# Optimization experiments

Measured on AMD Instinct MI355X. Metric: run time of the kernel, lower is better.

## Reference

```python
import jax, jax.numpy as jnp
import numpy as np

HEAD_DIM = 64


def rotate_half(x):
    x1, x2 = jnp.split(x, 2, axis=-1)
    return jnp.concatenate((-x2, x1), axis=-1)


def setup_inputs() -> dict:
    key = jax.random.key(0)
    ks = jax.random.split(key, 12)
    B, S, H, Hkv, D, hid = 1, 1536, 64, 8, HEAD_DIM, 2880
    std = 0.02
    x = jax.random.normal(ks[0], (B, S, hid), jnp.float32)
    # real RoPE cache, layout [cos | sin] of shape (S, 2*D)
    inv = 1.0 / (10000.0 ** (np.arange(0, D, 2, dtype=np.float32) / D))
    freqs = np.outer(np.arange(S, dtype=np.float32), inv)          # (S, D/2)
    emb = np.concatenate([freqs, freqs], axis=-1)                  # (S, D)
    rope_cache = jnp.asarray(
        np.concatenate([np.cos(emb), np.sin(emb)], axis=-1), jnp.float32
    )
    return {
        "x": x,
        "rope_cache": rope_cache,
        "wq_w": jax.random.normal(ks[1], (H * D, hid), jnp.float32) * std,
        "wq_b": jax.random.normal(ks[2], (H * D,), jnp.float32) * std,
        "wk_w": jax.random.normal(ks[3], (Hkv * D, hid), jnp.float32) * std,
        "wk_b": jax.random.normal(ks[4], (Hkv * D,), jnp.float32) * std,
        "wv_w": jax.random.normal(ks[5], (Hkv * D, hid), jnp.float32) * std,
        "wv_b": jax.random.normal(ks[6], (Hkv * D,), jnp.float32) * std,
        "wo_w": jax.random.normal(ks[7], (hid, H * D), jnp.float32) * std,
        "wo_b": jax.random.normal(ks[8], (hid,), jnp.float32) * std,
        "sinks": jax.random.normal(ks[9], (H,), jnp.float32) * std,
    }


def reference(x, rope_cache, wq_w, wq_b, wk_w, wk_b, wv_w, wv_b, wo_w, wo_b, sinks):
    B, S, hid = x.shape
    D = HEAD_DIM
    H = wq_w.shape[0] // D
    Hkv = wk_w.shape[0] // D
    n_rep = H // Hkv

    q = (x @ wq_w.T + wq_b).reshape(B, S, H, D)
    k = (x @ wk_w.T + wk_b).reshape(B, S, Hkv, D)
    v = (x @ wv_w.T + wv_b).reshape(B, S, Hkv, D)

    # RoPE (rotate-half form); rope_cache[:, :D]=cos, [:, D:]=sin
    cos = rope_cache[:S, :D][None, :, None, :]
    sin = rope_cache[:S, D:][None, :, None, :]
    q = q * cos + rotate_half(q) * sin
    k = k * cos + rotate_half(k) * sin

    # GQA repeat_kv: interleaved repeat along head dim
    k = jnp.repeat(k, n_rep, axis=2)  # (B, S, H, D)
    v = jnp.repeat(v, n_rep, axis=2)

    scale = 1.0 / jnp.sqrt(jnp.asarray(D, x.dtype))
    scores = jnp.einsum("bqhd,bkhd->bhqk", q, k) * scale  # (B, H, S, S)
    i = jnp.arange(S)
    causal = i[:, None] >= i[None, :]
    neg = jnp.asarray(jnp.finfo(scores.dtype).min, scores.dtype)
    scores = jnp.where(causal[None, None], scores, neg)

    lse = jax.nn.logsumexp(scores, axis=-1)               # (B, H, S)
    attn = jax.nn.softmax(scores, axis=-1)
    out = jnp.einsum("bhqk,bkhd->bqhd", attn, v)          # (B, S, H, D)

    # attention-sink rescale: sigmoid(lse - sink_logit)
    sink_scale = jax.nn.sigmoid(lse - sinks[None, :, None])  # (B, H, S)
    out = out * jnp.transpose(sink_scale, (0, 2, 1))[..., None]

    out = out.reshape(B, S, H * D)
    return out @ wo_w.T + wo_b
```

## Files before the change

kernel.cpp:

```cpp
#include <hip/hip_runtime.h>

typedef unsigned short u16;
typedef unsigned int u32;
typedef __attribute__((ext_vector_type(8))) __bf16 bf16x8;
typedef __attribute__((ext_vector_type(8))) u16 u16x8;
typedef __attribute__((ext_vector_type(4))) u16 u16x4;
typedef __attribute__((ext_vector_type(4))) float f32x4;
typedef __attribute__((ext_vector_type(2))) u32 u32x2;

#define DEV static __device__ __forceinline__

DEV u16 f2bf(float f) {
  unsigned u = __builtin_bit_cast(unsigned, f);
  u += 0x7FFFu + ((u >> 16) & 1u);
  return (u16)(u >> 16);
}

DEV float ex2(float x) { return __builtin_amdgcn_exp2f(x); }

DEV u32 cvt_pk_bf16(float lo, float hi) {
  u32 r;
  asm("v_cvt_pk_bf16_f32 %0, %1, %2" : "=v"(r) : "v"(lo), "v"(hi));
  return r;
}

DEV f32x4 mfma16(bf16x8 a, bf16x8 b, f32x4 c) {
  return __builtin_amdgcn_mfma_f32_16x16x32_bf16(a, b, c, 0, 0, 0);
}

DEV f32x4 fmax4(f32x4 a, f32x4 b) {
  f32x4 r;
  r[0] = fmaxf(a[0], b[0]); r[1] = fmaxf(a[1], b[1]);
  r[2] = fmaxf(a[2], b[2]); r[3] = fmaxf(a[3], b[3]);
  return r;
}

DEV void gload_lds16(const u16* g, u16* lds) {
  __builtin_amdgcn_global_load_lds(
      (const __attribute__((address_space(1))) void*)g,
      (__attribute__((address_space(3))) void*)lds, 16, 0, 0);
}

DEV void vm_wait4() { asm volatile("s_waitcnt vmcnt(4)" ::: "memory"); }
DEV void vm_wait2() { asm volatile("s_waitcnt vmcnt(2)" ::: "memory"); }
DEV void vm_wait0() { asm volatile("s_waitcnt vmcnt(0)" ::: "memory"); }

__global__ __launch_bounds__(256) void cvt_all(
    const float* __restrict__ x, const float* __restrict__ wq,
    const float* __restrict__ wk, const float* __restrict__ wv,
    const float* __restrict__ wo, const float* __restrict__ qb,
    const float* __restrict__ kb, const float* __restrict__ vb,
    u16* __restrict__ x_bf, u16* __restrict__ wqkv_bf,
    u16* __restrict__ wo_bf, float* __restrict__ bias_p) {
  const int NX = 1536 * 2880 / 8;
  const int NWQ = 4096 * 2880 / 8;
  const int NWKV = 512 * 2880 / 8;
  const int NWO = 3072 * 4096 / 8;
  const int C0 = NX, C1 = C0 + NWQ, C2 = C1 + NWKV, C3 = C2 + NWKV;
  const int C4 = C3 + NWO, C5 = C4 + 5120 / 8;
  int i = blockIdx.x * 256 + threadIdx.x;
  if (i >= C5) return;
  if (i < C4) {
    const float* s;
    u16* d;
    bool pad = false;
    if (i < C0) { s = x + (size_t)i * 8; d = x_bf + (size_t)i * 8; }
    else if (i < C1) { size_t q = i - C0; s = wq + q * 8; d = wqkv_bf + q * 8; }
    else if (i < C2) { size_t q = i - C1; s = wk + q * 8; d = wqkv_bf + (size_t)NWQ * 8 + q * 8; }
    else if (i < C3) { size_t q = i - C2; s = wv + q * 8; d = wqkv_bf + (size_t)(NWQ + NWKV) * 8 + q * 8; }
    else {
      size_t q = i - C3;
      int row = (int)(q >> 9);
      pad = (row >= 2880);
      s = wo + q * 8; d = wo_bf + q * 8;
    }
    u16x8 o;
    if (!pad) {
      float4 v0 = *(const float4*)s;
      float4 v1 = *(const float4*)(s + 4);
      o = (u16x8){f2bf(v0.x), f2bf(v0.y), f2bf(v0.z), f2bf(v0.w),
                  f2bf(v1.x), f2bf(v1.y), f2bf(v1.z), f2bf(v1.w)};
    } else {
      o = (u16x8){0, 0, 0, 0, 0, 0, 0, 0};
    }
    *(u16x8*)d = o;
  } else {
    int e = (i - C4) * 8;
#pragma unroll
    for (int j = 0; j < 8; j++) {
      int idx = e + j;
      bias_p[idx] = (idx < 4096) ? qb[idx] : (idx < 4608 ? kb[idx - 4096] : vb[idx - 4608]);
    }
  }
}

template <int MODE>
__global__ __launch_bounds__(512) void gemm128(const u16* __restrict__ A,
                                               const u16* __restrict__ B,
                                               const float* __restrict__ bias,
                                               float* __restrict__ C,
                                               u16* __restrict__ Obf,
                                               const float* __restrict__ rope,
                                               int M, int K, int Nreal, int ldc) {
  __shared__ u16 smA[2][128 * 64];
  __shared__ u16 smB[2][128 * 64];
  int nbm = M >> 7;
  int chunk = gridDim.x >> 3;
  int wg = (blockIdx.x & 7) * chunk + (blockIdx.x >> 3);
  int bm = wg % nbm, bn = wg / nbm;
  int t = threadIdx.x, lane = t & 63, wv = t >> 6;
  int wr = wv >> 1, wc = wv & 1;
  int l15 = lane & 15, hi = lane >> 4;
  f32x4 acc[2][4] = {};
  int tr = t >> 3;
  int scol = ((t & 7) ^ (tr & 7)) * 8;
  const u16* Ab = A + (size_t)(bm * 128 + tr) * K + scol;
  const u16* Bb = B + (size_t)(bn * 128 + tr) * K + scol;

  auto stage = [&](int b, int ks) {
    int k0 = ks * 64;
    gload_lds16(Ab + k0, &smA[b][t * 8]);
    gload_lds16(Ab + k0 + (size_t)64 * K, &smA[b][4096 + t * 8]);
    gload_lds16(Bb + k0, &smB[b][t * 8]);
    gload_lds16(Bb + k0 + (size_t)64 * K, &smB[b][4096 + t * 8]);
  };

  int NK = K >> 6;
  stage(0, 0);
  stage(1, 1);
  for (int ks = 0; ks < NK; ks++) {
    int cur = ks & 1;
    if (ks + 1 < NK) vm_wait4(); else vm_wait0();
    __builtin_amdgcn_s_barrier();
    __builtin_amdgcn_sched_barrier(0);
#pragma unroll
    for (int kk = 0; kk < 2; kk++) {
      int sc = ((kk * 4 + hi) ^ (l15 & 7)) * 8;
      bf16x8 af[2], bfr[4];
#pragma unroll
      for (int m = 0; m < 2; m++)
        af[m] = *(const bf16x8*)(&smA[cur][(wr * 32 + m * 16 + l15) * 64 + sc]);
#pragma unroll
      for (int n = 0; n < 4; n++)
        bfr[n] = *(const bf16x8*)(&smB[cur][(wc * 64 + n * 16 + l15) * 64 + sc]);
      __builtin_amdgcn_s_setprio(1);
#pragma unroll
      for (int m = 0; m < 2; m++)
#pragma unroll
        for (int n = 0; n < 4; n++)
          acc[m][n] = mfma16(af[m], bfr[n], acc[m][n]);
      __builtin_amdgcn_s_setprio(0);
    }
    __builtin_amdgcn_s_barrier();
    if (ks + 2 < NK) stage(cur, ks + 2);
  }

  int r0 = bm * 128 + wr * 32 + hi * 4;
  int c0 = bn * 128 + wc * 64 + l15;
  if (MODE == 0) {
#pragma unroll
    for (int n = 0; n < 4; n++) {
      int col = c0 + n * 16;
      if (col >= Nreal) continue;
      float bv = bias[col];
#pragma unroll
      for (int m = 0; m < 2; m++)
#pragma unroll
        for (int r = 0; r < 4; r++)
          C[(size_t)(r0 + m * 16 + r) * ldc + col] = acc[m][n][r] + bv;
    }
  } else {
    float bv[4];
#pragma unroll
    for (int n = 0; n < 4; n++) bv[n] = bias[c0 + n * 16];
    if (bn < 36) {
      float scale = (bn < 32) ? 0.180336880f : 1.0f;
#pragma unroll
      for (int m = 0; m < 2; m++) {
#pragma unroll
        for (int r = 0; r < 4; r++) {
          int s = r0 + m * 16 + r;
          const float* rp = rope + (size_t)s * 128;
          float cv0 = rp[l15], cv1 = rp[l15 + 16];
          float sv0 = rp[64 + l15], sv1 = rp[64 + l15 + 16];
          float v0 = acc[0][0][r], v1 = acc[0][1][r];
          float v2 = acc[0][2][r], v3 = acc[0][3][r];
          if (m) { v0 = acc[1][0][r]; v1 = acc[1][1][r]; v2 = acc[1][2][r]; v3 = acc[1][3][r]; }
          v0 += bv[0]; v1 += bv[1]; v2 += bv[2]; v3 += bv[3];
          u16* po = Obf + (size_t)s * 5120 + c0;
          po[0]  = f2bf((v0 * cv0 - v2 * sv0) * scale);
          po[16] = f2bf((v1 * cv1 - v3 * sv1) * scale);
          po[32] = f2bf((v2 * cv0 + v0 * sv0) * scale);
          po[48] = f2bf((v3 * cv1 + v1 * sv1) * scale);
        }
      }
    } else {
#pragma unroll
      for (int m = 0; m < 2; m++)
#pragma unroll
        for (int r = 0; r < 4; r++) {
          int s = r0 + m * 16 + r;
          u16* po = Obf + (size_t)s * 5120 + c0;
#pragma unroll
          for (int n = 0; n < 4; n++) po[n * 16] = f2bf(acc[m][n][r] + bv[n]);
        }
    }
  }
}

__global__ __launch_bounds__(256) void cast_trT(const u16* __restrict__ src,
                                                u16* __restrict__ dst, int S, int Hkv,
                                                int ld, int col0) {
  __shared__ u16 tile[64][65];
  int s0 = blockIdx.x * 64;
  int hkv = blockIdx.y;
  int t = threadIdx.x;
  int dl = (t & 15) * 4;
  int sl = t >> 4;
#pragma unroll
  for (int j = 0; j < 4; j++) {
    int s = sl + j * 16;
    u16x4 v = *(const u16x4*)(src + (size_t)(s0 + s) * ld + col0 + hkv * 64 + dl);
    tile[dl + 0][s] = v[0];
    tile[dl + 1][s] = v[1];
    tile[dl + 2][s] = v[2];
    tile[dl + 3][s] = v[3];
  }
  __syncthreads();
  int sl2 = (t & 7) * 8;
  int dl2 = t >> 3;
#pragma unroll
  for (int j = 0; j < 2; j++) {
    int d = dl2 + j * 32;
    u16x8 o;
#pragma unroll
    for (int c = 0; c < 8; c++) o[c] = tile[d][sl2 + c];
    *(u16x8*)(dst + ((size_t)hkv * 64 + d) * S + s0 + sl2) = o;
  }
}

__global__ __launch_bounds__(512) void attn_fwd(const u16* __restrict__ QKV,
                                                const u16* __restrict__ VT,
                                                const float* __restrict__ sinks,
                                                u16* __restrict__ Out,
                                                int S, int H, int Hkv) {
  __shared__ u16 ldsK[2][64 * 64];
  __shared__ u16 ldsV[2][64 * 64];
  __shared__ u16 ldsP[8][16 * 64];
  int bx = blockIdx.x, pair = blockIdx.y;
  int t = threadIdx.x, lane = t & 63, wv = t >> 6;
  int wq = wv & 3;
  int h = pair * 2 + (wv >> 2);
  int hkv = pair >> 2;
  int l15 = lane & 15, hi = lane >> 4;
  const u16* Kh = QKV + 4096 + hkv * 64;
  const u16* VTh = VT + (size_t)hkv * 64 * S;
  u16* ldsPw = &ldsP[wv][0];
  int psw = (l15 & 7) << 4;
  float snk = sinks[h];

  auto stage = [&](int b, int kb) {
    int k0 = kb * 64;
    int row = t >> 3, c16 = t & 7;
    int sc = (c16 ^ (row & 7)) * 8;
    gload_lds16(Kh + (size_t)(k0 + row) * 5120 + sc, &ldsK[b][t * 8]);
    gload_lds16(VTh + (size_t)row * S + k0 + sc, &ldsV[b][t * 8]);
  };

  for (int pass = 0; pass < 2; pass++) {
    int qb = pass == 0 ? (12 + bx) : (11 - bx);
    int q0 = qb * 64 + wq * 16;
    int rowq = q0 + l15;
    const u16* Qh = QKV + (size_t)q0 * 5120 + h * 64;
    bf16x8 qf[2];
    qf[0] = *(const bf16x8*)(Qh + (size_t)l15 * 5120 + hi * 8);
    qf[1] = *(const bf16x8*)(Qh + (size_t)l15 * 5120 + 32 + hi * 8);

    float mx = -1e30f, ls = 0.f;
    f32x4 ao[4] = {};

    int nkb = qb + 1;
    stage(0, 0);
    if (nkb > 1) stage(1, 1);
    for (int kb = 0; kb < nkb; kb++) {
      int cur = kb & 1;
      if (kb + 1 < nkb) vm_wait2(); else vm_wait0();
      __builtin_amdgcn_s_barrier();
      __builtin_amdgcn_sched_barrier(0);
      {
        f32x4 s[4] = {};
        __builtin_amdgcn_s_setprio(1);
#pragma unroll
        for (int kk = 0; kk < 2; kk++) {
#pragma unroll
          for (int ct = 0; ct < 4; ct++) {
            int row = ct * 16 + l15;
            int c16 = (kk * 4 + hi) ^ (row & 7);
            bf16x8 kf = *(const bf16x8*)(&ldsK[cur][row * 64 + c16 * 8]);
            s[ct] = mfma16(kf, qf[kk], s[ct]);
          }
        }
        __builtin_amdgcn_s_setprio(0);

        bool full = (kb * 64 + 63) < q0;
        if (!full) {
          int kc = kb * 64 + hi * 4;
#pragma unroll
          for (int ct = 0; ct < 4; ct++)
#pragma unroll
            for (int r = 0; r < 4; r++)
              if (kc + ct * 16 + r > rowq) s[ct][r] = -1e30f;
        }

        f32x4 mm = fmax4(fmax4(s[0], s[1]), fmax4(s[2], s[3]));
        float tmx = fmaxf(fmaxf(mm[0], mm[1]), fmaxf(mm[2], mm[3]));
        tmx = fmaxf(tmx, __shfl_xor(tmx, 16));
        tmx = fmaxf(tmx, __shfl_xor(tmx, 32));
        bool upd = __any(tmx > mx + 8.0f);
        if (upd) {
          float mn = fmaxf(mx, tmx);
          float al = ex2(mx - mn);
          mx = mn;
          ls *= al;
          float alr[4];
#pragma unroll
          for (int r = 0; r < 4; r++) alr[r] = __shfl(al, hi * 4 + r);
#pragma unroll
          for (int nt = 0; nt < 4; nt++)
#pragma unroll
            for (int r = 0; r < 4; r++) ao[nt][r] *= alr[r];
        }
#pragma unroll
        for (int ct = 0; ct < 4; ct++)
#pragma unroll
          for (int r = 0; r < 4; r++) s[ct][r] = ex2(s[ct][r] - mx);
        f32x4 sm = s[0] + s[1] + s[2] + s[3];
        float rs = (sm[0] + sm[1]) + (sm[2] + sm[3]);
        rs += __shfl_xor(rs, 16);
        rs += __shfl_xor(rs, 32);
        ls += rs;

#pragma unroll
        for (int ct = 0; ct < 4; ct++) {
          u32x2 pk = {cvt_pk_bf16(s[ct][0], s[ct][1]),
                      cvt_pk_bf16(s[ct][2], s[ct][3])};
          *(u32x2*)(&ldsPw[(l15 * 128 + ((ct * 32 + hi * 8) ^ psw)) >> 1]) = pk;
        }

        __builtin_amdgcn_s_setprio(1);
#pragma unroll
        for (int kk = 0; kk < 2; kk++) {
          bf16x8 pa = *(const bf16x8*)(&ldsPw[(l15 * 128 + ((kk * 64 + hi * 16) ^ psw)) >> 1]);
#pragma unroll
          for (int nt = 0; nt < 4; nt++) {
            int vrow = nt * 16 + l15;
            int c16 = (kk * 4 + hi) ^ (vrow & 7);
            bf16x8 vf = *(const bf16x8*)(&ldsV[cur][vrow * 64 + c16 * 8]);
            ao[nt] = mfma16(pa, vf, ao[nt]);
          }
        }
        __builtin_amdgcn_s_setprio(0);
      }
      __builtin_amdgcn_s_barrier();
      if (kb + 2 < nkb) stage(cur, kb + 2);
    }

    float lse = 0.69314718056f * mx + __logf(ls);
    float ss = 1.f / (1.f + __expf(snk - lse));
    float f = ss / ls;
    float fr[4];
#pragma unroll
    for (int r = 0; r < 4; r++) fr[r] = __shfl(f, hi * 4 + r);
#pragma unroll
    for (int r = 0; r < 4; r++) {
      int row = q0 + hi * 4 + r;
#pragma unroll
      for (int nt = 0; nt < 4; nt++)
        Out[(size_t)row * (H * 64) + h * 64 + nt * 16 + l15] = f2bf(ao[nt][r] * fr[r]);
    }
  }
}

extern "C" void kernel_launch(void* const* d_in, const int* in_sizes, int n_in,
                              void* d_out, int out_size, void* d_ws, size_t ws_size,
                              hipStream_t stream) {
  const int S = 1536, HID = 2880, H = 64, HKV = 8;
  const int NQ = 4096, NKV = 512, NQKV = 5120, NPAD = 3072;

  const float* x     = (const float*)d_in[0];
  const float* rope  = (const float*)d_in[1];
  const float* wq_w  = (const float*)d_in[2];
  const float* wq_b  = (const float*)d_in[3];
  const float* wk_w  = (const float*)d_in[4];
  const float* wk_b  = (const float*)d_in[5];
  const float* wv_w  = (const float*)d_in[6];
  const float* wv_b  = (const float*)d_in[7];
  const float* wo_w  = (const float*)d_in[8];
  const float* wo_b  = (const float*)d_in[9];
  const float* sinks = (const float*)d_in[10];
  float* out = (float*)d_out;

  char* ws = (char*)d_ws;
  size_t off = 0;
  auto alloc = [&](size_t bytes) {
    char* p = ws + off;
    off = (off + bytes + 255) & ~(size_t)255;
    return p;
  };
  u16*   x_bf    = (u16*)  alloc((size_t)S * HID * 2);
  u16*   wqkv_bf = (u16*)  alloc((size_t)NQKV * HID * 2);
  u16*   wo_bf   = (u16*)  alloc((size_t)NPAD * NQ * 2);
  u16*   qkv_bf  = (u16*)  alloc((size_t)S * NQKV * 2);
  float* bias_p  = (float*)alloc((size_t)NQKV * 4);
  u16*   VTb     = (u16*)  alloc((size_t)HKV * 64 * S * 2);
  u16*   att     = (u16*)  alloc((size_t)S * NQ * 2);
  (void)ws_size; (void)n_in; (void)in_sizes; (void)out_size;

  auto cdiv = [](int a, int b) { return (a + b - 1) / b; };

  const int NCVT = (S * HID + NQ * HID + 2 * (NKV * HID) + NPAD * NQ + NQKV) / 8;
  cvt_all<<<cdiv(NCVT, 256), 256, 0, stream>>>(x, wq_w, wk_w, wv_w, wo_w,
                                               wq_b, wk_b, wv_b,
                                               x_bf, wqkv_bf, wo_bf, bias_p);

  gemm128<1><<<(S / 128) * (NQKV / 128), 512, 0, stream>>>(
      x_bf, wqkv_bf, bias_p, nullptr, qkv_bf, rope, S, HID, NQKV, NQKV);

  cast_trT<<<dim3(S / 64, HKV), 256, 0, stream>>>(qkv_bf, VTb, S, HKV, NQKV, NQ + NKV);

  attn_fwd<<<dim3(12, H / 2), 512, 0, stream>>>(qkv_bf, VTb, sinks, att, S, H, HKV);

  gemm128<0><<<(S / 128) * (NPAD / 128), 512, 0, stream>>>(
      att, wo_bf, wo_b, out, nullptr, nullptr, S, NQ, HID, HID);
}
```

Before: 186.7 us.

## Load GEMM A-operand fragments directly from global into registers, dropping A LDS staging

The 128x128 GEMM no longer stages the A tile in shared memory. Each wave loads its own A fragments from global memory straight into registers, one k-step ahead, while B stays double-buffered in LDS through global_load_lds. The vmcnt wait threshold is raised to account for the extra in-flight register loads. This halves LDS traffic and footprint, at the cost of uncoalesced per-lane global reads of A, duplicated across the two column waves, plus more registers for prefetched fragments.

```diff
diff --git a/kernel.cpp b/kernel.cpp
--- a/kernel.cpp
+++ b/kernel.cpp
@@ -41,7 +41,7 @@
       (__attribute__((address_space(3))) void*)lds, 16, 0, 0);
 }
 
-DEV void vm_wait4() { asm volatile("s_waitcnt vmcnt(4)" ::: "memory"); }
+DEV void vm_wait6() { asm volatile("s_waitcnt vmcnt(6)" ::: "memory"); }
 DEV void vm_wait2() { asm volatile("s_waitcnt vmcnt(2)" ::: "memory"); }
 DEV void vm_wait0() { asm volatile("s_waitcnt vmcnt(0)" ::: "memory"); }
 
@@ -102,7 +102,6 @@
                                                u16* __restrict__ Obf,
                                                const float* __restrict__ rope,
                                                int M, int K, int Nreal, int ldc) {
-  __shared__ u16 smA[2][128 * 64];
   __shared__ u16 smB[2][128 * 64];
   int nbm = M >> 7;
   int chunk = gridDim.x >> 3;
@@ -114,45 +113,73 @@
   f32x4 acc[2][4] = {};
   int tr = t >> 3;
   int scol = ((t & 7) ^ (tr & 7)) * 8;
-  const u16* Ab = A + (size_t)(bm * 128 + tr) * K + scol;
   const u16* Bb = B + (size_t)(bn * 128 + tr) * K + scol;
-
-  auto stage = [&](int b, int ks) {
+  const u16* Ar = A + (size_t)(bm * 128 + wr * 32 + l15) * K + hi * 8;
+  const size_t AM = (size_t)16 * K;
+
+  auto stageB = [&](int b, int ks) {
     int k0 = ks * 64;
-    gload_lds16(Ab + k0, &smA[b][t * 8]);
-    gload_lds16(Ab + k0 + (size_t)64 * K, &smA[b][4096 + t * 8]);
     gload_lds16(Bb + k0, &smB[b][t * 8]);
     gload_lds16(Bb + k0 + (size_t)64 * K, &smB[b][4096 + t * 8]);
   };
 
   int NK = K >> 6;
-  stage(0, 0);
-  stage(1, 1);
+  stageB(0, 0);
+  stageB(1, 1);
+  bf16x8 ac0 = *(const bf16x8*)(Ar);
+  bf16x8 ac1 = *(const bf16x8*)(Ar + AM);
+  bf16x8 ac2 = *(const bf16x8*)(Ar + 32);
+  bf16x8 ac3 = *(const bf16x8*)(Ar + AM + 32);
   for (int ks = 0; ks < NK; ks++) {
     int cur = ks & 1;
-    if (ks + 1 < NK) vm_wait4(); else vm_wait0();
+    if (ks + 1 < NK) vm_wait6(); else vm_wait0();
     __builtin_amdgcn_s_barrier();
     __builtin_amdgcn_sched_barrier(0);
-#pragma unroll
-    for (int kk = 0; kk < 2; kk++) {
-      int sc = ((kk * 4 + hi) ^ (l15 & 7)) * 8;
-      bf16x8 af[2], bfr[4];
-#pragma unroll
-      for (int m = 0; m < 2; m++)
-        af[m] = *(const bf16x8*)(&smA[cur][(wr * 32 + m * 16 + l15) * 64 + sc]);
-#pragma unroll
-      for (int n = 0; n < 4; n++)
-        bfr[n] = *(const bf16x8*)(&smB[cur][(wc * 64 + n * 16 + l15) * 64 + sc]);
+    bf16x8 an0, an1, an2, an3;
+    if (ks + 1 < NK) {
+      int kn = (ks + 1) * 64;
+      an0 = *(const bf16x8*)(Ar + kn);
+      an1 = *(const bf16x8*)(Ar + AM + kn);
+      an2 = *(const bf16x8*)(Ar + kn + 32);
+      an3 = *(const bf16x8*)(Ar + AM + kn + 32);
+    }
+    {
+      int sc = (hi ^ (l15 & 7)) * 8;
+      bf16x8 b0 = *(const bf16x8*)(&smB[cur][(wc * 64 + 0 * 16 + l15) * 64 + sc]);
+      bf16x8 b1 = *(const bf16x8*)(&smB[cur][(wc * 64 + 1 * 16 + l15) * 64 + sc]);
+      bf16x8 b2 = *(const bf16x8*)(&smB[cur][(wc * 64 + 2 * 16 + l15) * 64 + sc]);
+      bf16x8 b3 = *(const bf16x8*)(&smB[cur][(wc * 64 + 3 * 16 + l15) * 64 + sc]);
       __builtin_amdgcn_s_setprio(1);
-#pragma unroll
-      for (int m = 0; m < 2; m++)
-#pragma unroll
-        for (int n = 0; n < 4; n++)
-          acc[m][n] = mfma16(af[m], bfr[n], acc[m][n]);
+      acc[0][0] = mfma16(ac0, b0, acc[0][0]);
+      acc[0][1] = mfma16(ac0, b1, acc[0][1]);
+      acc[0][2] = mfma16(ac0, b2, acc[0][2]);
+      acc[0][3] = mfma16(ac0, b3, acc[0][3]);
+      acc[1][0] = mfma16(ac1, b0, acc[1][0]);
+      acc[1][1] = mfma16(ac1, b1, acc[1][1]);
+      acc[1][2] = mfma16(ac1, b2, acc[1][2]);
+      acc[1][3] = mfma16(ac1, b3, acc[1][3]);
       __builtin_amdgcn_s_setprio(0);
     }
+    {
+      int sc = ((4 + hi) ^ (l15 & 7)) * 8;
+      bf16x8 b0 = *(const bf16x8*)(&smB[cur][(wc * 64 + 0 * 16 + l15) * 64 + sc]);
+      bf16x8 b1 = *(const bf16x8*)(&smB[cur][(wc * 64 + 1 * 16 + l15) * 64 + sc]);
+      bf16x8 b2 = *(const bf16x8*)(&smB[cur][(wc * 64 + 2 * 16 + l15) * 64 + sc]);
+      bf16x8 b3 = *(const bf16x8*)(&smB[cur][(wc * 64 + 3 * 16 + l15) * 64 + sc]);
+      __builtin_amdgcn_s_setprio(1);
+      acc[0][0] = mfma16(ac2, b0, acc[0][0]);
+      acc[0][1] = mfma16(ac2, b1, acc[0][1]);
+      acc[0][2] = mfma16(ac2, b2, acc[0][2]);
+      acc[0][3] = mfma16(ac2, b3, acc[0][3]);
+      acc[1][0] = mfma16(ac3, b0, acc[1][0]);
+      acc[1][1] = mfma16(ac3, b1, acc[1][1]);
+      acc[1][2] = mfma16(ac3, b2, acc[1][2]);
+      acc[1][3] = mfma16(ac3, b3, acc[1][3]);
+      __builtin_amdgcn_s_setprio(0);
+    }
     __builtin_amdgcn_s_barrier();
-    if (ks + 2 < NK) stage(cur, ks + 2);
+    if (ks + 2 < NK) stageB(cur, ks + 2);
+    if (ks + 1 < NK) { ac0 = an0; ac1 = an1; ac2 = an2; ac3 = an3; }
   }
 
   int r0 = bm * 128 + wr * 32 + hi * 4;
```

Result: slower. 305.6 us (+63.7%).

## Split-K the output projection GEMM into two partials plus a reduction kernel

Applied to the files above, without the earlier changes.

The output projection GEMM gets a new mode that splits K into two halves along grid y. Each half writes fp32 partial sums into a scratch buffer that reuses the x_bf workspace region, and a new reduce kernel adds the two partials plus bias into the output. The aim is to double the number of workgroups so the GPU's compute units fill better and the last-wave tail shrinks. In exchange it writes and reads about 38 MB of fp32 partials and adds an extra kernel launch. The scratch buffer also overruns x_bf into the wqkv_bf region, which is only safe because that buffer is dead by this point.

```diff
diff --git a/kernel.cpp b/kernel.cpp
--- a/kernel.cpp
+++ b/kernel.cpp
@@ -114,8 +114,14 @@
   f32x4 acc[2][4] = {};
   int tr = t >> 3;
   int scol = ((t & 7) ^ (tr & 7)) * 8;
-  const u16* Ab = A + (size_t)(bm * 128 + tr) * K + scol;
-  const u16* Bb = B + (size_t)(bn * 128 + tr) * K + scol;
+  int NK = K >> 6;
+  size_t koff = 0;
+  if (MODE == 2) {
+    NK >>= 1;
+    koff = (size_t)blockIdx.y * (NK << 6);
+  }
+  const u16* Ab = A + (size_t)(bm * 128 + tr) * K + scol + koff;
+  const u16* Bb = B + (size_t)(bn * 128 + tr) * K + scol + koff;
 
   auto stage = [&](int b, int ks) {
     int k0 = ks * 64;
@@ -125,7 +131,6 @@
     gload_lds16(Bb + k0 + (size_t)64 * K, &smB[b][4096 + t * 8]);
   };
 
-  int NK = K >> 6;
   stage(0, 0);
   stage(1, 1);
   for (int ks = 0; ks < NK; ks++) {
@@ -168,6 +173,17 @@
 #pragma unroll
         for (int r = 0; r < 4; r++)
           C[(size_t)(r0 + m * 16 + r) * ldc + col] = acc[m][n][r] + bv;
+    }
+  } else if (MODE == 2) {
+    float* Cp = C + (size_t)blockIdx.y * M * ldc;
+#pragma unroll
+    for (int n = 0; n < 4; n++) {
+      int col = c0 + n * 16;
+#pragma unroll
+      for (int m = 0; m < 2; m++)
+#pragma unroll
+        for (int r = 0; r < 4; r++)
+          Cp[(size_t)(r0 + m * 16 + r) * ldc + col] = acc[m][n][r];
     }
   } else {
     float bv[4];
@@ -206,6 +222,23 @@
         }
     }
   }
+}
+
+__global__ __launch_bounds__(256) void reduce_wo(const float* __restrict__ p,
+                                                 const float* __restrict__ bias,
+                                                 float* __restrict__ out) {
+  const int QPR = 2880 / 4;
+  int i = blockIdx.x * 256 + threadIdx.x;
+  if (i >= 1536 * QPR) return;
+  int row = i / QPR, c4 = (i - row * QPR) * 4;
+  const float* a0 = p + (size_t)row * 3072 + c4;
+  const float* a1 = a0 + (size_t)1536 * 3072;
+  float4 v0 = *(const float4*)a0;
+  float4 v1 = *(const float4*)a1;
+  float4 b = *(const float4*)(bias + c4);
+  float4 o = {v0.x + v1.x + b.x, v0.y + v1.y + b.y,
+              v0.z + v1.z + b.z, v0.w + v1.w + b.w};
+  *(float4*)(out + (size_t)row * 2880 + c4) = o;
 }
 
 __global__ __launch_bounds__(256) void cast_trT(const u16* __restrict__ src,
@@ -414,6 +447,7 @@
   float* bias_p  = (float*)alloc((size_t)NQKV * 4);
   u16*   VTb     = (u16*)  alloc((size_t)HKV * 64 * S * 2);
   u16*   att     = (u16*)  alloc((size_t)S * NQ * 2);
+  float* wo_part = (float*)x_bf;
   (void)ws_size; (void)n_in; (void)in_sizes; (void)out_size;
 
   auto cdiv = [](int a, int b) { return (a + b - 1) / b; };
@@ -430,6 +464,7 @@
 
   attn_fwd<<<dim3(12, H / 2), 512, 0, stream>>>(qkv_bf, VTb, sinks, att, S, H, HKV);
 
-  gemm128<0><<<(S / 128) * (NPAD / 128), 512, 0, stream>>>(
-      att, wo_bf, wo_b, out, nullptr, nullptr, S, NQ, HID, HID);
-}
+  gemm128<2><<<dim3((S / 128) * (NPAD / 128), 2), 512, 0, stream>>>(
+      att, wo_bf, nullptr, wo_part, nullptr, nullptr, S, NQ, HID, NPAD);
+  reduce_wo<<<cdiv(S * HID / 4, 256), 256, 0, stream>>>(wo_part, wo_b, out);
+}
```

After: 196.2 us. 1.05x slower.
